# Performance work log

Hardware: AMD Instinct MI355X
Metric: run time of the kernel (lower is better)

## Reference

```python
import jax, jax.numpy as jnp
import numpy as np

# ---- static hyperparams (from comp_encoding.__init__ / DMPNNEncoderLayer) ----
B = 512            # number of molecules in the batch (wrapper's python loop)
A = 128            # padded atoms per molecule == max_mol_len
E = 256            # padded directed bonds per molecule
K = 6              # max incoming bonds gathered per bond/atom
ATOM_FDIM = 133
BOND_FDIM = 14
H = 128            # d_hidden = max_mol_len
DEPTH = 3
G = 2048           # global feature dim (Morgan fingerprint)


def _mol_lens():
    ml = np.array(jax.random.randint(jax.random.fold_in(jax.random.key(0), 5), (B,), 16, H + 1))
    ml[0] = H  # ensure comp_dim == max(mol_lens) == H so per-row padding is a no-op
    return ml


def setup_inputs() -> dict:
    key = jax.random.key(0)
    ks = jax.random.split(key, 10)
    atom_feature = jax.random.normal(ks[0], (B, A, ATOM_FDIM), jnp.float32)
    f_ini_atoms_bond = jax.random.normal(ks[1], (B, E, ATOM_FDIM + BOND_FDIM), jnp.float32)
    atom_to_incoming_bond = jax.random.randint(ks[2], (B, A, K), 0, E)
    mapping = jax.random.randint(ks[3], (B, E, K), 0, E)
    global_f = jax.random.normal(ks[4], (B, G), jnp.float32)
    mol_lens = _mol_lens()  # static numpy ints (constants, drive output shapes)
    W_i = jax.random.normal(ks[6], (H, ATOM_FDIM + BOND_FDIM), jnp.float32) / np.float32(np.sqrt(ATOM_FDIM + BOND_FDIM))
    W_h = jax.random.normal(ks[7], (H, H), jnp.float32) / np.float32(np.sqrt(H))
    W_o = jax.random.normal(ks[8], (H, ATOM_FDIM + H), jnp.float32) / np.float32(np.sqrt(ATOM_FDIM + H))
    b_o = jax.random.normal(ks[9], (H,), jnp.float32) * 0.01
    return dict(atom_feature=atom_feature, f_ini_atoms_bond=f_ini_atoms_bond,
                atom_to_incoming_bond=atom_to_incoming_bond, mapping=mapping,
                global_f=global_f, mol_lens=mol_lens,
                W_i=W_i, W_h=W_h, W_o=W_o, b_o=b_o)


def _gather_sum(msg, idx):
    # msg: [B, E, H]; idx: [B, N, K] -> sum over K incoming messages: [B, N, H]
    b, n, k = idx.shape
    g = jnp.take_along_axis(msg, idx.reshape(b, n * k)[..., None], axis=1)
    return g.reshape(b, n, k, -1).sum(axis=2)


def reference(atom_feature, f_ini_atoms_bond, atom_to_incoming_bond, mapping,
              global_f, mol_lens, W_i, W_h, W_o, b_o):
    # DMPNN: W_i on initial directed-bond features
    inp = jnp.einsum('bef,hf->beh', f_ini_atoms_bond, W_i)   # [B, E, H]
    msg = jax.nn.relu(inp)
    for _ in range(DEPTH - 1):
        agg = _gather_sum(msg, mapping)                      # [B, E, H]
        msg = jax.nn.relu(inp + jnp.einsum('beh,gh->beg', agg, W_h))
    m2a = _gather_sum(msg, atom_to_incoming_bond)            # [B, A, H]
    cat = jnp.concatenate([atom_feature, m2a], axis=-1)      # [B, A, 133+H]
    atoms_h = jax.nn.relu(jnp.einsum('bad,hd->bah', cat, W_o) + b_o)  # [B, A, H]

    # wrapper: take first mol_len atom encodings per molecule, stack, build mask
    ml = np.asarray(mol_lens)
    valid = np.arange(A)[None, :] < ml[:, None]              # [B, A] static
    b_idx, a_idx = np.nonzero(valid)
    comp = atoms_h[b_idx, a_idx]                             # [sum(mol_lens), H]
    c_mask = jnp.asarray(valid.astype(np.float32))           # [B, comp_dim]
    return comp, c_mask
```

## Files before the change

kernel.cpp:

```cpp
#include <hip/hip_runtime.h>

typedef unsigned int   uint;
typedef unsigned short ushort;
typedef short bf16x8 __attribute__((ext_vector_type(8)));
typedef float f32x4  __attribute__((ext_vector_type(4)));

constexpr int Bm   = 512;
constexpr int Aa   = 128;
constexpr int Ee   = 256;
constexpr int Kk   = 6;
constexpr int AFD  = 133;
constexpr int FD   = 147;
constexpr int Hh   = 128;
constexpr int CATD = 261;
constexpr int KWI  = 192;
constexpr int KWO  = 320;
constexpr int MST  = 136;
constexpr int SST  = 72;

__device__ __forceinline__ ushort f2b(float f) {
    uint u = __float_as_uint(f);
    u += 0x7FFFu + ((u >> 16) & 1u);
    return (ushort)(u >> 16);
}
__device__ __forceinline__ uint f2b2(float x, float y) {
    return (uint)f2b(x) | ((uint)f2b(y) << 16);
}
__device__ __forceinline__ float2 b2f2(uint p) {
    float2 r;
    r.x = __uint_as_float(p << 16);
    r.y = __uint_as_float(p & 0xFFFF0000u);
    return r;
}

__device__ __forceinline__ bf16x8 gsum6(const ushort* src, const int* mr, int ko) {
    float2 s0 = {0.f, 0.f}, s1 = {0.f, 0.f}, s2 = {0.f, 0.f}, s3 = {0.f, 0.f};
#pragma unroll
    for (int k = 0; k < Kk; ++k) {
        uint4 m = *(const uint4*)&src[mr[k] + ko];
        float2 a = b2f2(m.x); s0.x += a.x; s0.y += a.y;
        float2 b = b2f2(m.y); s1.x += b.x; s1.y += b.y;
        float2 d = b2f2(m.z); s2.x += d.x; s2.y += d.y;
        float2 e = b2f2(m.w); s3.x += e.x; s3.y += e.y;
    }
    uint4 o;
    o.x = f2b2(s0.x, s0.y); o.y = f2b2(s1.x, s1.y);
    o.z = f2b2(s2.x, s2.y); o.w = f2b2(s3.x, s3.y);
    bf16x8 r;
    __builtin_memcpy(&r, &o, 16);
    return r;
}

__global__ __launch_bounds__(256) void k_prep_w(const float* __restrict__ Wi,
                                                const float* __restrict__ Wh,
                                                const float* __restrict__ Wo,
                                                ushort* __restrict__ Wi_b,
                                                ushort* __restrict__ Wh_b,
                                                ushort* __restrict__ Wo_b) {
    const int h = blockIdx.x, t = threadIdx.x;
    for (int c = t; c < KWI; c += 256)
        Wi_b[h * KWI + c] = f2b(c < FD ? Wi[h * FD + c] : 0.f);
    for (int c = t; c < Hh; c += 256)
        Wh_b[h * Hh + c] = f2b(Wh[h * Hh + c]);
    for (int c = t; c < KWO; c += 256) {
        float v = 0.f;
        if (c < AFD)       v = Wo[h * CATD + c];
        else if (c >= 192) v = Wo[h * CATD + AFD + (c - 192)];
        Wo_b[h * KWO + c] = f2b(v);
    }
}

__global__ __launch_bounds__(512) void k_scan(const int* __restrict__ ml,
                                              int* __restrict__ pfx) {
    __shared__ int s[512];
    int t = threadIdx.x;
    s[t] = ml[t];
    __syncthreads();
    for (int off = 1; off < 512; off <<= 1) {
        int v = (t >= off) ? s[t - off] : 0;
        __syncthreads();
        s[t] += v;
        __syncthreads();
    }
    pfx[t + 1] = s[t];
    if (t == 0) pfx[0] = 0;
}

__global__ __launch_bounds__(512, 2) void k_fused(
        const float* __restrict__ atomf,
        const float* __restrict__ fini,
        const int*   __restrict__ a2ib,
        const int*   __restrict__ mapping,
        const ushort* __restrict__ Wi_b,
        const ushort* __restrict__ Wh_b,
        const ushort* __restrict__ Wo_b,
        const float* __restrict__ bo,
        const int*   __restrict__ mol_lens,
        const int*   __restrict__ pfx,
        float* __restrict__ out,
        float* __restrict__ cmask) {
    __shared__ ushort msg0[Ee * MST];
    __shared__ ushort msg1[Ee * MST];
    __shared__ int    map_s[Ee * Kk];
    __shared__ int    a2_s[Aa * Kk];

    const int b    = blockIdx.x;
    const int tid  = threadIdx.x;
    const int wave = tid >> 6;
    const int lane = tid & 63;
    const int l15  = lane & 15, quad = lane >> 4;

    for (int i = tid; i < Ee * Kk; i += 512) map_s[i] = mapping[b * Ee * Kk + i];
    for (int i = tid; i < Aa * Kk; i += 512) a2_s[i]  = a2ib[b * Aa * Kk + i];
    const int len = mol_lens[b];
    if (tid < Aa) cmask[b * Aa + tid] = (tid < len) ? 1.0f : 0.0f;

    f32x4 acc[2][8];
#pragma unroll
    for (int i = 0; i < 2; ++i)
#pragma unroll
        for (int j = 0; j < 8; ++j) acc[i][j] = (f32x4){0.f, 0.f, 0.f, 0.f};

    const float* fsrc = fini + (size_t)b * Ee * FD;
    for (int c = 0; c < 3; ++c) {
        for (int idx = tid; idx < Ee * 16; idx += 512) {
            int r = idx >> 4, gg = idx & 15;
            int c0 = c * 64 + gg * 4;
            const float* sp = fsrc + (size_t)r * FD + c0;
            float v0 = (c0 + 0 < FD) ? sp[0] : 0.f;
            float v1 = (c0 + 1 < FD) ? sp[1] : 0.f;
            float v2 = (c0 + 2 < FD) ? sp[2] : 0.f;
            float v3 = (c0 + 3 < FD) ? sp[3] : 0.f;
            uint2 p;
            p.x = f2b2(v0, v1);
            p.y = f2b2(v2, v3);
            *(uint2*)&msg1[r * SST + gg * 4] = p;
        }
        __syncthreads();
#pragma unroll
        for (int ks = 0; ks < 2; ++ks) {
            const int ko = ks * 32 + quad * 8;
            bf16x8 bf[8], af[2];
#pragma unroll
            for (int j = 0; j < 8; ++j)
                bf[j] = *(const bf16x8*)&Wi_b[(j * 16 + l15) * KWI + c * 64 + ko];
#pragma unroll
            for (int i = 0; i < 2; ++i)
                af[i] = *(const bf16x8*)&msg1[(wave * 32 + i * 16 + l15) * SST + ko];
#pragma unroll
            for (int i = 0; i < 2; ++i)
#pragma unroll
                for (int j = 0; j < 8; ++j)
                    acc[i][j] = __builtin_amdgcn_mfma_f32_16x16x32_bf16(
                        af[i], bf[j], acc[i][j], 0, 0, 0);
        }
        __syncthreads();
    }

    uint2 inp_pk[2][8];
#pragma unroll
    for (int i = 0; i < 2; ++i)
#pragma unroll
        for (int j = 0; j < 8; ++j) {
            f32x4 a4 = acc[i][j];
            uint2 p;
            p.x = f2b2(a4[0], a4[1]);
            p.y = f2b2(a4[2], a4[3]);
            inp_pk[i][j] = p;
            int col = j * 16 + l15;
#pragma unroll
            for (int reg = 0; reg < 4; ++reg) {
                int row = wave * 32 + i * 16 + quad * 4 + reg;
                float v = a4[reg] > 0.f ? a4[reg] : 0.f;
                msg0[row * MST + col] = f2b(v);
            }
        }
    __syncthreads();

#pragma unroll
    for (int h = 0; h < 2; ++h) {
        const ushort* src = h ? msg1 : msg0;
        ushort*       dst = h ? msg0 : msg1;
        int mr[2][Kk];
#pragma unroll
        for (int i = 0; i < 2; ++i) {
            int row = wave * 32 + i * 16 + l15;
#pragma unroll
            for (int k = 0; k < Kk; ++k) mr[i][k] = map_s[row * Kk + k] * MST;
        }
#pragma unroll
        for (int i = 0; i < 2; ++i)
#pragma unroll
            for (int j = 0; j < 8; ++j) acc[i][j] = (f32x4){0.f, 0.f, 0.f, 0.f};
#pragma unroll
        for (int ks = 0; ks < 4; ++ks) {
            const int ko = ks * 32 + quad * 8;
            bf16x8 bf[8], af[2];
#pragma unroll
            for (int j = 0; j < 8; ++j)
                bf[j] = *(const bf16x8*)&Wh_b[(j * 16 + l15) * Hh + ko];
#pragma unroll
            for (int i = 0; i < 2; ++i) af[i] = gsum6(src, mr[i], ko);
#pragma unroll
            for (int i = 0; i < 2; ++i)
#pragma unroll
                for (int j = 0; j < 8; ++j)
                    acc[i][j] = __builtin_amdgcn_mfma_f32_16x16x32_bf16(
                        af[i], bf[j], acc[i][j], 0, 0, 0);
        }
#pragma unroll
        for (int i = 0; i < 2; ++i)
#pragma unroll
            for (int j = 0; j < 8; ++j) {
                float2 lo = b2f2(inp_pk[i][j].x);
                float2 hi = b2f2(inp_pk[i][j].y);
                float v[4];
                v[0] = lo.x + acc[i][j][0];
                v[1] = lo.y + acc[i][j][1];
                v[2] = hi.x + acc[i][j][2];
                v[3] = hi.y + acc[i][j][3];
                int col = j * 16 + l15;
#pragma unroll
                for (int reg = 0; reg < 4; ++reg) {
                    int row = wave * 32 + i * 16 + quad * 4 + reg;
                    float r = v[reg] > 0.f ? v[reg] : 0.f;
                    dst[row * MST + col] = f2b(r);
                }
            }
        __syncthreads();
    }

    f32x4 ro[8];
#pragma unroll
    for (int j = 0; j < 8; ++j) ro[j] = (f32x4){0.f, 0.f, 0.f, 0.f};

    const float* asrc = atomf + (size_t)b * Aa * AFD;
    for (int c = 0; c < 3; ++c) {
        for (int idx = tid; idx < Aa * 16; idx += 512) {
            int r = idx >> 4, gg = idx & 15;
            int c0 = c * 64 + gg * 4;
            const float* sp = asrc + (size_t)r * AFD + c0;
            float v0 = (c0 + 0 < AFD) ? sp[0] : 0.f;
            float v1 = (c0 + 1 < AFD) ? sp[1] : 0.f;
            float v2 = (c0 + 2 < AFD) ? sp[2] : 0.f;
            float v3 = (c0 + 3 < AFD) ? sp[3] : 0.f;
            uint2 p;
            p.x = f2b2(v0, v1);
            p.y = f2b2(v2, v3);
            *(uint2*)&msg1[r * SST + gg * 4] = p;
        }
        __syncthreads();
#pragma unroll
        for (int ks = 0; ks < 2; ++ks) {
            const int ko = ks * 32 + quad * 8;
            bf16x8 a0 = *(const bf16x8*)&msg1[(wave * 16 + l15) * SST + ko];
            bf16x8 bf[8];
#pragma unroll
            for (int j = 0; j < 8; ++j)
                bf[j] = *(const bf16x8*)&Wo_b[(j * 16 + l15) * KWO + c * 64 + ko];
#pragma unroll
            for (int j = 0; j < 8; ++j)
                ro[j] = __builtin_amdgcn_mfma_f32_16x16x32_bf16(a0, bf[j], ro[j], 0, 0, 0);
        }
        __syncthreads();
    }
    {
        int ar[Kk];
        int row = wave * 16 + l15;
#pragma unroll
        for (int k = 0; k < Kk; ++k) ar[k] = a2_s[row * Kk + k] * MST;
#pragma unroll
        for (int ks = 0; ks < 4; ++ks) {
            const int ko = ks * 32 + quad * 8;
            bf16x8 a0 = gsum6(msg0, ar, ko);
            bf16x8 bf[8];
#pragma unroll
            for (int j = 0; j < 8; ++j)
                bf[j] = *(const bf16x8*)&Wo_b[(j * 16 + l15) * KWO + 192 + ko];
#pragma unroll
            for (int j = 0; j < 8; ++j)
                ro[j] = __builtin_amdgcn_mfma_f32_16x16x32_bf16(a0, bf[j], ro[j], 0, 0, 0);
        }
    }

    const int base = pfx[b];
#pragma unroll
    for (int j = 0; j < 8; ++j) {
        int col = j * 16 + l15;
        float bv = bo[col];
#pragma unroll
        for (int reg = 0; reg < 4; ++reg) {
            int a = wave * 16 + quad * 4 + reg;
            if (a < len) {
                float v = ro[j][reg] + bv;
                out[(size_t)(base + a) * Hh + col] = v > 0.f ? v : 0.f;
            }
        }
    }
}

extern "C" void kernel_launch(void* const* d_in, const int* in_sizes, int n_in,
                              void* d_out, int out_size, void* d_ws, size_t ws_size,
                              hipStream_t stream) {
    const float* atom_feature = (const float*)d_in[0];
    const float* f_ini        = (const float*)d_in[1];
    const int*   a2ib         = (const int*)d_in[2];
    const int*   mapping      = (const int*)d_in[3];
    const int*   mol_lens     = (const int*)d_in[5];
    const float* Wi           = (const float*)d_in[6];
    const float* Wh           = (const float*)d_in[7];
    const float* Wo           = (const float*)d_in[8];
    const float* bo           = (const float*)d_in[9];
    float* out = (float*)d_out;

    ushort* Wi_b = (ushort*)d_ws;
    ushort* Wh_b = Wi_b + 128 * KWI;
    ushort* Wo_b = Wh_b + 128 * Hh;
    int*    pfx  = (int*)(Wo_b + 128 * KWO);

    float* cmask = out + ((size_t)out_size - (size_t)Bm * Aa);

    k_prep_w<<<128, 256, 0, stream>>>(Wi, Wh, Wo, Wi_b, Wh_b, Wo_b);
    k_scan  <<<1, 512, 0, stream>>>(mol_lens, pfx);
    k_fused <<<Bm, 512, 0, stream>>>(atom_feature, f_ini, a2ib, mapping,
                                     Wi_b, Wh_b, Wo_b, bo, mol_lens, pfx,
                                     out, cmask);
}
```

Before: 287.5 us.

## Single-buffer message LDS, load f32 inputs directly into MFMA fragments, raise occupancy

Replaces the double-buffered message arrays in LDS with one buffer, using an extra barrier between the gather reads and the in-place write-back. Initial bond and atom features are now loaded from global memory straight into bf16 MFMA fragments instead of being staged through LDS with barriers. The input projection is folded into the accumulator init, map indices are hoisted out of the depth loop, and launch bounds ask for 4 blocks per CU. Roughly halving LDS use allows higher occupancy, at the cost of uncoalesced per-lane global loads and more register pressure under the tighter bound.

```diff
diff --git a/kernel.cpp b/kernel.cpp
--- a/kernel.cpp
+++ b/kernel.cpp
@@ -1,4 +1,5 @@
 #include <hip/hip_runtime.h>
+#include <hip/hip_bf16.h>
 
 typedef unsigned int   uint;
 typedef unsigned short ushort;
@@ -16,15 +17,16 @@
 constexpr int KWI  = 192;
 constexpr int KWO  = 320;
 constexpr int MST  = 136;
-constexpr int SST  = 72;
 
 __device__ __forceinline__ ushort f2b(float f) {
     uint u = __float_as_uint(f);
     u += 0x7FFFu + ((u >> 16) & 1u);
     return (ushort)(u >> 16);
 }
-__device__ __forceinline__ uint f2b2(float x, float y) {
-    return (uint)f2b(x) | ((uint)f2b(y) << 16);
+__device__ __forceinline__ uint cvt2(float x, float y) {
+    float2 t2; t2.x = x; t2.y = y;
+    __hip_bfloat162 t = __float22bfloat162_rn(t2);
+    uint r; __builtin_memcpy(&r, &t, 4); return r;
 }
 __device__ __forceinline__ float2 b2f2(uint p) {
     float2 r;
@@ -44,8 +46,20 @@
         float2 e = b2f2(m.w); s3.x += e.x; s3.y += e.y;
     }
     uint4 o;
-    o.x = f2b2(s0.x, s0.y); o.y = f2b2(s1.x, s1.y);
-    o.z = f2b2(s2.x, s2.y); o.w = f2b2(s3.x, s3.y);
+    o.x = cvt2(s0.x, s0.y); o.y = cvt2(s1.x, s1.y);
+    o.z = cvt2(s2.x, s2.y); o.w = cvt2(s3.x, s3.y);
+    bf16x8 r;
+    __builtin_memcpy(&r, &o, 16);
+    return r;
+}
+
+__device__ __forceinline__ bf16x8 ld_frag_f32(const float* sp, int c0, int lim) {
+    float v[8];
+#pragma unroll
+    for (int d = 0; d < 8; ++d) v[d] = (c0 + d < lim) ? sp[d] : 0.f;
+    uint4 o;
+    o.x = cvt2(v[0], v[1]); o.y = cvt2(v[2], v[3]);
+    o.z = cvt2(v[4], v[5]); o.w = cvt2(v[6], v[7]);
     bf16x8 r;
     __builtin_memcpy(&r, &o, 16);
     return r;
@@ -86,7 +100,7 @@
     if (t == 0) pfx[0] = 0;
 }
 
-__global__ __launch_bounds__(512, 2) void k_fused(
+__global__ __launch_bounds__(512, 4) void k_fused(
         const float* __restrict__ atomf,
         const float* __restrict__ fini,
         const int*   __restrict__ a2ib,
@@ -99,8 +113,7 @@
         const int*   __restrict__ pfx,
         float* __restrict__ out,
         float* __restrict__ cmask) {
-    __shared__ ushort msg0[Ee * MST];
-    __shared__ ushort msg1[Ee * MST];
+    __shared__ ushort msg[Ee * MST];
     __shared__ int    map_s[Ee * Kk];
     __shared__ int    a2_s[Aa * Kk];
 
@@ -122,31 +135,20 @@
         for (int j = 0; j < 8; ++j) acc[i][j] = (f32x4){0.f, 0.f, 0.f, 0.f};
 
     const float* fsrc = fini + (size_t)b * Ee * FD;
+#pragma unroll
     for (int c = 0; c < 3; ++c) {
-        for (int idx = tid; idx < Ee * 16; idx += 512) {
-            int r = idx >> 4, gg = idx & 15;
-            int c0 = c * 64 + gg * 4;
-            const float* sp = fsrc + (size_t)r * FD + c0;
-            float v0 = (c0 + 0 < FD) ? sp[0] : 0.f;
-            float v1 = (c0 + 1 < FD) ? sp[1] : 0.f;
-            float v2 = (c0 + 2 < FD) ? sp[2] : 0.f;
-            float v3 = (c0 + 3 < FD) ? sp[3] : 0.f;
-            uint2 p;
-            p.x = f2b2(v0, v1);
-            p.y = f2b2(v2, v3);
-            *(uint2*)&msg1[r * SST + gg * 4] = p;
-        }
-        __syncthreads();
 #pragma unroll
         for (int ks = 0; ks < 2; ++ks) {
-            const int ko = ks * 32 + quad * 8;
-            bf16x8 bf[8], af[2];
-#pragma unroll
-            for (int j = 0; j < 8; ++j)
-                bf[j] = *(const bf16x8*)&Wi_b[(j * 16 + l15) * KWI + c * 64 + ko];
-#pragma unroll
-            for (int i = 0; i < 2; ++i)
-                af[i] = *(const bf16x8*)&msg1[(wave * 32 + i * 16 + l15) * SST + ko];
+            const int c0 = c * 64 + ks * 32 + quad * 8;
+            bf16x8 af[2], bf[8];
+#pragma unroll
+            for (int i = 0; i < 2; ++i) {
+                const int row = wave * 32 + i * 16 + l15;
+                af[i] = ld_frag_f32(fsrc + (size_t)row * FD + c0, c0, FD);
+            }
+#pragma unroll
+            for (int j = 0; j < 8; ++j)
+                bf[j] = *(const bf16x8*)&Wi_b[(j * 16 + l15) * KWI + c0];
 #pragma unroll
             for (int i = 0; i < 2; ++i)
 #pragma unroll
@@ -154,7 +156,6 @@
                     acc[i][j] = __builtin_amdgcn_mfma_f32_16x16x32_bf16(
                         af[i], bf[j], acc[i][j], 0, 0, 0);
         }
-        __syncthreads();
     }
 
     uint2 inp_pk[2][8];
@@ -164,43 +165,46 @@
         for (int j = 0; j < 8; ++j) {
             f32x4 a4 = acc[i][j];
             uint2 p;
-            p.x = f2b2(a4[0], a4[1]);
-            p.y = f2b2(a4[2], a4[3]);
+            p.x = cvt2(a4[0], a4[1]);
+            p.y = cvt2(a4[2], a4[3]);
             inp_pk[i][j] = p;
             int col = j * 16 + l15;
 #pragma unroll
             for (int reg = 0; reg < 4; ++reg) {
                 int row = wave * 32 + i * 16 + quad * 4 + reg;
                 float v = a4[reg] > 0.f ? a4[reg] : 0.f;
-                msg0[row * MST + col] = f2b(v);
+                msg[row * MST + col] = f2b(v);
             }
         }
     __syncthreads();
 
+    int mr[2][Kk];
+#pragma unroll
+    for (int i = 0; i < 2; ++i) {
+        int row = wave * 32 + i * 16 + l15;
+#pragma unroll
+        for (int k = 0; k < Kk; ++k) mr[i][k] = map_s[row * Kk + k] * MST;
+    }
+
 #pragma unroll
     for (int h = 0; h < 2; ++h) {
-        const ushort* src = h ? msg1 : msg0;
-        ushort*       dst = h ? msg0 : msg1;
-        int mr[2][Kk];
-#pragma unroll
-        for (int i = 0; i < 2; ++i) {
-            int row = wave * 32 + i * 16 + l15;
-#pragma unroll
-            for (int k = 0; k < Kk; ++k) mr[i][k] = map_s[row * Kk + k] * MST;
-        }
 #pragma unroll
         for (int i = 0; i < 2; ++i)
 #pragma unroll
-            for (int j = 0; j < 8; ++j) acc[i][j] = (f32x4){0.f, 0.f, 0.f, 0.f};
+            for (int j = 0; j < 8; ++j) {
+                float2 lo = b2f2(inp_pk[i][j].x);
+                float2 hi = b2f2(inp_pk[i][j].y);
+                acc[i][j] = (f32x4){lo.x, lo.y, hi.x, hi.y};
+            }
 #pragma unroll
         for (int ks = 0; ks < 4; ++ks) {
             const int ko = ks * 32 + quad * 8;
-            bf16x8 bf[8], af[2];
+            bf16x8 af[2], bf[8];
+#pragma unroll
+            for (int i = 0; i < 2; ++i) af[i] = gsum6(msg, mr[i], ko);
 #pragma unroll
             for (int j = 0; j < 8; ++j)
                 bf[j] = *(const bf16x8*)&Wh_b[(j * 16 + l15) * Hh + ko];
-#pragma unroll
-            for (int i = 0; i < 2; ++i) af[i] = gsum6(src, mr[i], ko);
 #pragma unroll
             for (int i = 0; i < 2; ++i)
 #pragma unroll
@@ -208,23 +212,17 @@
                     acc[i][j] = __builtin_amdgcn_mfma_f32_16x16x32_bf16(
                         af[i], bf[j], acc[i][j], 0, 0, 0);
         }
+        __syncthreads();
 #pragma unroll
         for (int i = 0; i < 2; ++i)
 #pragma unroll
             for (int j = 0; j < 8; ++j) {
-                float2 lo = b2f2(inp_pk[i][j].x);
-                float2 hi = b2f2(inp_pk[i][j].y);
-                float v[4];
-                v[0] = lo.x + acc[i][j][0];
-                v[1] = lo.y + acc[i][j][1];
-                v[2] = hi.x + acc[i][j][2];
-                v[3] = hi.y + acc[i][j][3];
                 int col = j * 16 + l15;
 #pragma unroll
                 for (int reg = 0; reg < 4; ++reg) {
                     int row = wave * 32 + i * 16 + quad * 4 + reg;
-                    float r = v[reg] > 0.f ? v[reg] : 0.f;
-                    dst[row * MST + col] = f2b(r);
+                    float v = acc[i][j][reg];
+                    msg[row * MST + col] = f2b(v > 0.f ? v : 0.f);
                 }
             }
         __syncthreads();
@@ -234,49 +232,37 @@
 #pragma unroll
     for (int j = 0; j < 8; ++j) ro[j] = (f32x4){0.f, 0.f, 0.f, 0.f};
 
-    const float* asrc = atomf + (size_t)b * Aa * AFD;
-    for (int c = 0; c < 3; ++c) {
-        for (int idx = tid; idx < Aa * 16; idx += 512) {
-            int r = idx >> 4, gg = idx & 15;
-            int c0 = c * 64 + gg * 4;
-            const float* sp = asrc + (size_t)r * AFD + c0;
-            float v0 = (c0 + 0 < AFD) ? sp[0] : 0.f;
-            float v1 = (c0 + 1 < AFD) ? sp[1] : 0.f;
-            float v2 = (c0 + 2 < AFD) ? sp[2] : 0.f;
-            float v3 = (c0 + 3 < AFD) ? sp[3] : 0.f;
-            uint2 p;
-            p.x = f2b2(v0, v1);
-            p.y = f2b2(v2, v3);
-            *(uint2*)&msg1[r * SST + gg * 4] = p;
-        }
-        __syncthreads();
-#pragma unroll
-        for (int ks = 0; ks < 2; ++ks) {
-            const int ko = ks * 32 + quad * 8;
-            bf16x8 a0 = *(const bf16x8*)&msg1[(wave * 16 + l15) * SST + ko];
-            bf16x8 bf[8];
-#pragma unroll
-            for (int j = 0; j < 8; ++j)
-                bf[j] = *(const bf16x8*)&Wo_b[(j * 16 + l15) * KWO + c * 64 + ko];
-#pragma unroll
-            for (int j = 0; j < 8; ++j)
-                ro[j] = __builtin_amdgcn_mfma_f32_16x16x32_bf16(a0, bf[j], ro[j], 0, 0, 0);
-        }
-        __syncthreads();
-    }
     {
         int ar[Kk];
-        int row = wave * 16 + l15;
+        const int row = wave * 16 + l15;
 #pragma unroll
         for (int k = 0; k < Kk; ++k) ar[k] = a2_s[row * Kk + k] * MST;
 #pragma unroll
         for (int ks = 0; ks < 4; ++ks) {
             const int ko = ks * 32 + quad * 8;
-            bf16x8 a0 = gsum6(msg0, ar, ko);
+            bf16x8 a0 = gsum6(msg, ar, ko);
             bf16x8 bf[8];
 #pragma unroll
             for (int j = 0; j < 8; ++j)
                 bf[j] = *(const bf16x8*)&Wo_b[(j * 16 + l15) * KWO + 192 + ko];
+#pragma unroll
+            for (int j = 0; j < 8; ++j)
+                ro[j] = __builtin_amdgcn_mfma_f32_16x16x32_bf16(a0, bf[j], ro[j], 0, 0, 0);
+        }
+    }
+
+    const float* asrc = atomf + (size_t)b * Aa * AFD;
+#pragma unroll
+    for (int c = 0; c < 3; ++c) {
+#pragma unroll
+        for (int ks = 0; ks < 2; ++ks) {
+            const int c0 = c * 64 + ks * 32 + quad * 8;
+            const int row = wave * 16 + l15;
+            bf16x8 a0 = ld_frag_f32(asrc + (size_t)row * AFD + c0, c0, AFD);
+            bf16x8 bf[8];
+#pragma unroll
+            for (int j = 0; j < 8; ++j)
+                bf[j] = *(const bf16x8*)&Wo_b[(j * 16 + l15) * KWO + c0];
 #pragma unroll
             for (int j = 0; j < 8; ++j)
                 ro[j] = __builtin_amdgcn_mfma_f32_16x16x32_bf16(a0, bf[j], ro[j], 0, 0, 0);
```

After: 381.6 us. 1.33x slower.
